# Kernel tuning notes

Hardware: AMD Instinct MI355X
Metric: run time of the kernel (lower is better)

Reference implementation:

```python
import jax, jax.numpy as jnp
import numpy as np

S, B, E, H, Q, T, K, N = 256, 32, 768, 1024, 64, 512, 11, 16
STD = 2.5
EPS = 1e-5


def gaussian_kernel(size, std):
    t = np.linspace(-(size - 1) / 2, (size - 1) / 2, size)
    x, y = np.meshgrid(t, t)
    kern = np.exp(-0.5 * (x ** 2 + y ** 2) / std ** 2)
    return (kern / kern.sum()).astype(np.float32)


def setup_inputs() -> dict:
    key = jax.random.key(0)
    ks = jax.random.split(key, 24)
    s = 0.05
    inp = {
        'sentence_batch': jax.random.normal(ks[0], (S, B, E), jnp.float32),
        # forward LSTM params (torch layout: W_ih (4H,E), W_hh (4H,H), gate order i,f,g,o)
        'Wih_f': jax.random.normal(ks[1], (4 * H, E), jnp.float32) * s,
        'Whh_f': jax.random.normal(ks[2], (4 * H, H), jnp.float32) * s,
        'bih_f': jnp.zeros((4 * H,), jnp.float32),
        'bhh_f': jnp.zeros((4 * H,), jnp.float32),
        # backward LSTM params
        'Wih_b': jax.random.normal(ks[3], (4 * H, E), jnp.float32) * s,
        'Whh_b': jax.random.normal(ks[4], (4 * H, H), jnp.float32) * s,
        'bih_b': jnp.zeros((4 * H,), jnp.float32),
        'bhh_b': jnp.zeros((4 * H,), jnp.float32),
        # layer norms
        'g_in': jnp.ones((E,), jnp.float32), 'be_in': jnp.zeros((E,), jnp.float32),
        'g_fw': jnp.ones((H,), jnp.float32), 'be_fw': jnp.zeros((H,), jnp.float32),
        'g_bk': jnp.ones((H,), jnp.float32), 'be_bk': jnp.zeros((H,), jnp.float32),
        'g_sq': jnp.ones((2 * Q,), jnp.float32), 'be_sq': jnp.zeros((2 * Q,), jnp.float32),
        # squeeze + topic linears (torch layout: W (out,in))
        'Wsq': jax.random.normal(ks[5], (Q, H), jnp.float32) * s,
        'bsq': jnp.zeros((Q,), jnp.float32),
        'Wtop': jax.random.normal(ks[6], (T, 2 * Q), jnp.float32) * s,
        'btop': jnp.zeros((T,), jnp.float32),
        'gauss_kern': jnp.asarray(gaussian_kernel(K, STD)),
    }
    return inp


def layer_norm(x, g, b):
    mu = jnp.mean(x, axis=-1, keepdims=True)
    var = jnp.mean((x - mu) ** 2, axis=-1, keepdims=True)
    return g * (x - mu) * jax.lax.rsqrt(var + EPS) + b


def lstm(x, Wih, Whh, bih, bhh):
    # x: (S, B, E) -> hidden states (S, B, H). torch gate order: i, f, g, o.
    h0 = jnp.zeros((x.shape[1], Whh.shape[1]), x.dtype)
    c0 = jnp.zeros_like(h0)
    xg = jnp.einsum('sbe,ge->sbg', x, Wih) + bih  # precompute input gates

    def step(carry, xt):
        h, c = carry
        gates = xt + h @ Whh.T + bhh
        i, f, g, o = jnp.split(gates, 4, axis=-1)
        c = jax.nn.sigmoid(f) * c + jax.nn.sigmoid(i) * jnp.tanh(g)
        h = jax.nn.sigmoid(o) * jnp.tanh(c)
        return (h, c), h

    _, hs = jax.lax.scan(step, (h0, c0), xg)
    return hs


def batch_pca(e, dim):
    # e: (S, B, F) -> projections (B, S, dim) onto top-dim principal axes
    c = e - jnp.mean(e, axis=0)
    cov = jnp.einsum('sbi,sbj->bij', c, c) / e.shape[0]  # (B, F, F), symmetric
    _, evecs = jnp.linalg.eigh(cov)  # ascending eigenvalues
    top = evecs[:, :, ::-1][:, :, :dim]  # (B, F, dim), descending order
    return jnp.einsum('sbf,bfn->bsn', c, top)


def gauss_smooth(x, kern):
    # x: (B, S, N) smoothed with 2D gaussian, SAME padding
    p = (kern.shape[0] - 1) // 2
    y = jax.lax.conv_general_dilated(
        x[:, None, :, :], kern[None, None, :, :], (1, 1), [(p, p), (p, p)])
    return y[:, 0]


def adj_cos(e):
    # cosine similarity between adjacent sequence positions: (B, S, N) -> (B, S-1)
    a, b = e[:, :-1], e[:, 1:]
    num = jnp.sum(a * b, axis=-1)
    den = jnp.linalg.norm(a, axis=-1) * jnp.linalg.norm(b, axis=-1)
    return num / den


def reference(sentence_batch, Wih_f, Whh_f, bih_f, bhh_f, Wih_b, Whh_b, bih_b, bhh_b,
              g_in, be_in, g_fw, be_fw, g_bk, be_bk, g_sq, be_sq,
              Wsq, bsq, Wtop, btop, gauss_kern):
    x = layer_norm(sentence_batch, g_in, be_in)
    x_f = lstm(x, Wih_f, Whh_f, bih_f, bhh_f)
    x_b = lstm(x[::-1], Wih_b, Whh_b, bih_b, bhh_b)[::-1]
    x_f = layer_norm(x_f, g_fw, be_fw)
    x_b = layer_norm(x_b, g_bk, be_bk)
    x_f = jnp.tanh(jnp.einsum('sbh,qh->sbq', x_f, Wsq) + bsq)
    x_b = jnp.tanh(jnp.einsum('sbh,qh->sbq', x_b, Wsq) + bsq)
    xc = layer_norm(jnp.concatenate((x_f, x_b), axis=-1), g_sq, be_sq)
    topic_preds = jnp.einsum('sbq,tq->sbt', xc, Wtop) + btop

    # segmentation path (no-grad in original)
    e_f = batch_pca(jax.lax.stop_gradient(x_f), N)
    e_b = batch_pca(jax.lax.stop_gradient(x_b), N)
    e_f = gauss_smooth(e_f, gauss_kern)
    e_b = gauss_smooth(e_b, gauss_kern)
    d = jnp.sqrt(adj_cos(e_f) * adj_cos(e_b))  # (B, S-1)
    pos = jnp.argmax(d, axis=1)
    return topic_preds, pos
```

## Files before the change

kernel.cpp:

```cpp
#include <hip/hip_runtime.h>
#include <cstdint>
#include <cstddef>

#define SS   256
#define BB   32
#define EE   768
#define HH   1024
#define QQ   64
#define TTOP 512
#define NPC  16
#define G4   4096
#define TCHUNK 32
#define NBLK 256
#define EPSF 1e-5f

#define OFF_XNT   ((size_t)0)
#define OFF_WHHT  ((size_t)6291456)
#define OFF_CT    ((size_t)14680064)
#define OFF_HBUF  ((size_t)14745600)
#define OFF_CNT   ((size_t)14876672)
#define OFF_XG    ((size_t)14877184)
#define OFF_HS    ((size_t)23265792)
#define OFF_XQ    ((size_t)40043008)
#define OFF_CMAT  ((size_t)0)
#define OFF_COV   ((size_t)1048576)
#define OFF_PG    ((size_t)1310720)
#define OFF_COS   ((size_t)1376256)

#define WLKS 4616
#define LSTM_DYN_LDS 153344

#define AST 65
#define EIG_DYN_LDS 133120

#define EPS32D    5.9604644775390625e-8
#define EPS232D   (EPS32D*EPS32D)
#define SAFMIN32D 1.1754943508222875e-38

__device__ __forceinline__ float sigm(float x){ return 1.0f/(1.0f + expf(-x)); }

__device__ __forceinline__ double wsumd(double v){
  #pragma unroll
  for (int o = 32; o; o >>= 1) v += __shfl_xor(v, o, 64);
  return v;
}
__device__ __forceinline__ double wmaxd(double v){
  #pragma unroll
  for (int o = 32; o; o >>= 1) v = fmax(v, __shfl_xor(v, o, 64));
  return v;
}
__device__ __forceinline__ void dlartg_(double f, double g, double& c, double& s, double& r){
  if (g == 0.0){ c = 1.0; s = 0.0; r = f; }
  else if (f == 0.0){ c = 0.0; s = (g >= 0.0) ? 1.0 : -1.0; r = fabs(g); }
  else {
    double d = sqrt(f*f + g*g);
    c = fabs(f)/d;
    r = copysign(d, f);
    s = g/r;
  }
}
__device__ void dlaev2_(double a, double b, double c,
                        double& rt1, double& rt2, double& cs1, double& sn1){
  double sm = a + c, df = a - c, adf = fabs(df), tb = b + b, ab = fabs(tb);
  double acmx, acmn;
  if (fabs(a) > fabs(c)){ acmx = a; acmn = c; } else { acmx = c; acmn = a; }
  double rt;
  if (adf > ab)      rt = adf*sqrt(1.0 + (ab/adf)*(ab/adf));
  else if (adf < ab) rt = ab*sqrt(1.0 + (adf/ab)*(adf/ab));
  else               rt = ab*sqrt(2.0);
  int sgn1;
  if (sm < 0.0){ rt1 = 0.5*(sm - rt); sgn1 = -1; rt2 = (acmx/rt1)*acmn - (b/rt1)*b; }
  else if (sm > 0.0){ rt1 = 0.5*(sm + rt); sgn1 = 1; rt2 = (acmx/rt1)*acmn - (b/rt1)*b; }
  else { rt1 = 0.5*rt; rt2 = -0.5*rt; sgn1 = 1; }
  double cs; int sgn2;
  if (df >= 0.0){ cs = df + rt; sgn2 = 1; } else { cs = df - rt; sgn2 = -1; }
  double acs = fabs(cs);
  if (acs > ab){ double ct = -tb/cs; sn1 = 1.0/sqrt(1.0+ct*ct); cs1 = ct*sn1; }
  else {
    if (ab == 0.0){ cs1 = 1.0; sn1 = 0.0; }
    else { double tn = -cs/tb; cs1 = 1.0/sqrt(1.0+tn*tn); sn1 = tn*cs1; }
  }
  if (sgn1 == sgn2){ double tn = cs1; cs1 = -sn1; sn1 = tn; }
}

__device__ void dsteqr16_(int base, double* d, double* e, double* z16, int ln){
  if (ln < 16){
    #pragma unroll
    for (int j = 0; j < 16; j++) z16[ln*17+j] = (ln==j) ? 1.0 : 0.0;
  }
  const int n = 16, nm1 = 15;
  int jtot = 0; const int nmaxit = 480;
  int l1 = 0;
  while (l1 < n){
    if (l1 > 0) e[base+l1-1] = 0.0;
    int m = nm1;
    for (int mm = l1; mm < nm1; mm++){
      double tst = fabs(e[base+mm]);
      if (tst == 0.0){ m = mm; break; }
      if (tst <= (sqrt(fabs(d[base+mm]))*sqrt(fabs(d[base+mm+1])))*EPS32D){
        e[base+mm] = 0.0; m = mm; break;
      }
    }
    int l = l1, lend = m;
    l1 = m + 1;
    if (lend == l) continue;
    if (fabs(d[base+lend]) < fabs(d[base+l])){ int t = l; l = lend; lend = t; }
    if (lend > l){
      for (;;){
        int mm = lend;
        for (int k2 = l; k2 < lend; k2++){
          double tst = e[base+k2]*e[base+k2];
          if (tst <= (EPS232D*fabs(d[base+k2]))*fabs(d[base+k2+1]) + SAFMIN32D){ mm = k2; break; }
        }
        if (mm < lend) e[base+mm] = 0.0;
        double p = d[base+l];
        if (mm == l){ l++; if (l <= lend) continue; break; }
        if (mm == l+1){
          double rt1, rt2, cc, ss;
          dlaev2_(d[base+l], e[base+l], d[base+l+1], rt1, rt2, cc, ss);
          if (ln < 16){
            double x = z16[ln*17+l], y = z16[ln*17+l+1];
            z16[ln*17+l]   = cc*x + ss*y;
            z16[ln*17+l+1] = cc*y - ss*x;
          }
          d[base+l] = rt1; d[base+l+1] = rt2; e[base+l] = 0.0;
          l += 2; if (l <= lend) continue; break;
        }
        if (jtot == nmaxit) break;
        jtot++;
        double g = (d[base+l+1]-p)/(2.0*e[base+l]);
        double r = sqrt(g*g+1.0);
        g = d[base+mm] - p + e[base+l]/(g + copysign(r, g));
        double s2 = 1.0, c2 = 1.0; p = 0.0;
        for (int i = mm-1; i >= l; i--){
          double f = s2*e[base+i], b = c2*e[base+i];
          dlartg_(g, f, c2, s2, r);
          if (i != mm-1) e[base+i+1] = r;
          g = d[base+i+1] - p;
          r = (d[base+i]-g)*s2 + 2.0*c2*b;
          p = s2*r;
          d[base+i+1] = g + p;
          g = c2*r - b;
          if (ln < 16){
            double x = z16[ln*17+i], y = z16[ln*17+i+1];
            z16[ln*17+i]   = c2*x - s2*y;
            z16[ln*17+i+1] = s2*x + c2*y;
          }
        }
        d[base+l] -= p; e[base+l] = g;
      }
    } else {
      for (;;){
        int mm = lend;
        for (int k2 = l; k2 > lend; k2--){
          double tst = e[base+k2-1]*e[base+k2-1];
          if (tst <= (EPS232D*fabs(d[base+k2]))*fabs(d[base+k2-1]) + SAFMIN32D){ mm = k2; break; }
        }
        if (mm > lend) e[base+mm-1] = 0.0;
        double p = d[base+l];
        if (mm == l){ l--; if (l >= lend) continue; break; }
        if (mm == l-1){
          double rt1, rt2, cc, ss;
          dlaev2_(d[base+l-1], e[base+l-1], d[base+l], rt1, rt2, cc, ss);
          if (ln < 16){
            double x = z16[ln*17+l-1], y = z16[ln*17+l];
            z16[ln*17+l-1] = cc*x + ss*y;
            z16[ln*17+l]   = cc*y - ss*x;
          }
          d[base+l-1] = rt1; d[base+l] = rt2; e[base+l-1] = 0.0;
          l -= 2; if (l >= lend) continue; break;
        }
        if (jtot == nmaxit) break;
        jtot++;
        double g = (d[base+l-1]-p)/(2.0*e[base+l-1]);
        double r = sqrt(g*g+1.0);
        g = d[base+mm] - p + e[base+l-1]/(g + copysign(r, g));
        double s2 = 1.0, c2 = 1.0; p = 0.0;
        for (int i = mm; i <= l-1; i++){
          double f = s2*e[base+i], b = c2*e[base+i];
          dlartg_(g, f, c2, s2, r);
          if (i != mm) e[base+i-1] = r;
          g = d[base+i] - p;
          r = (d[base+i+1]-g)*s2 + 2.0*c2*b;
          p = s2*r;
          d[base+i] = g + p;
          g = c2*r - b;
          if (ln < 16){
            double x = z16[ln*17+i], y = z16[ln*17+i+1];
            z16[ln*17+i]   = c2*x + s2*y;
            z16[ln*17+i+1] = c2*y - s2*x;
          }
        }
        d[base+l] -= p; e[base+l-1] = g;
      }
    }
  }
  for (int ii = 1; ii < n; ii++){
    int i = ii-1, k = i; double p = d[base+i];
    for (int j = ii; j < n; j++) if (d[base+j] < p){ k = j; p = d[base+j]; }
    if (k != i){
      d[base+k] = d[base+i]; d[base+i] = p;
      if (ln < 16){ double t = z16[ln*17+i]; z16[ln*17+i] = z16[ln*17+k]; z16[ln*17+k] = t; }
    }
  }
}

__device__ void dc_merge(int base, int n1, int n2, double rho_in, int tid,
    double* s_d, double* Zt, double* Tt,
    double* md, double* mz, double* dl, double* wz, double* lam, double* zh,
    double* ev, double* su4, int* indx, int* sec, int* defl, int* prm,
    int* sKn){
  const int ln = tid & 63, w = tid >> 6;
  int n = n1 + n2;
  double zv = 0.0;
  if (ln < n){
    if (ln < n1) zv = Zt[(size_t)(base+n1-1)*AST + base + ln];
    else         zv = Zt[(size_t)(base+n1)*AST + base + ln];
    if (rho_in < 0.0 && ln >= n1) zv = -zv;
  }
  zv *= 0.70710678118654752440;
  mz[ln] = (ln < n) ? zv : 0.0;
  md[ln] = (ln < n) ? s_d[base+ln] : 0.0;
  __syncthreads();
  double rho = fabs(2.0*rho_in);
  if (tid == 0){
    int i1 = 0, i2 = n1, k = 0;
    while (i1 < n1 && i2 < n){
      if (md[i2] < md[i1]) indx[k++] = i2++; else indx[k++] = i1++;
    }
    while (i1 < n1) indx[k++] = i1++;
    while (i2 < n)  indx[k++] = i2++;
  }
  __syncthreads();
  double dmax = wmaxd((ln<n) ? fabs(md[ln]) : 0.0);
  double zmax = wmaxd((ln<n) ? fabs(mz[ln]) : 0.0);
  double tol = 8.0*EPS32D*fmax(dmax, zmax);
  if (w == 0){
    int K = 0, ndefl = 0, pj = -1;
    for (int j = 0; j < n; j++){
      int nj = indx[j];
      if (rho*fabs(mz[nj]) <= tol){
        defl[ndefl++] = nj;
      } else if (pj < 0){
        pj = nj;
      } else {
        double sG = mz[pj], cG = mz[nj];
        double tau = sqrt(cG*cG + sG*sG);
        double tdf = md[nj] - md[pj];
        double c = cG/tau, s = -sG/tau;
        if (fabs(tdf*c*s) <= tol){
          mz[nj] = tau; mz[pj] = 0.0;
          if (ln < n){
            double x = Zt[(size_t)(base+ln)*AST + base+pj];
            double y = Zt[(size_t)(base+ln)*AST + base+nj];
            Zt[(size_t)(base+ln)*AST + base+pj] = c*x + s*y;
            Zt[(size_t)(base+ln)*AST + base+nj] = c*y - s*x;
          }
          double t2 = md[pj]*c*c + md[nj]*s*s;
          double t3 = md[pj]*s*s + md[nj]*c*c;
          md[nj] = t3; md[pj] = t2;
          defl[ndefl++] = pj;
          pj = nj;
        } else {
          sec[K] = pj; dl[K] = md[pj]; wz[K] = mz[pj]; K++;
          pj = nj;
        }
      }
    }
    if (pj >= 0){ sec[K] = pj; dl[K] = md[pj]; wz[K] = mz[pj]; K++; }
    if (ln == 0){ sKn[0] = K; sKn[1] = ndefl; }
  }
  __syncthreads();
  const int K = sKn[0], ndefl = sKn[1];
  double wsum2 = wsumd((ln < K) ? wz[ln]*wz[ln] : 0.0);
  {
    bool conv = (ln >= K);
    double lo = 0.0, hi = 0.0;
    if (!conv){
      lo = dl[ln];
      hi = (ln < K-1) ? dl[ln+1] : (dl[K-1] + rho*wsum2);
    }
    const int i2lo = w*16;
    for (int it = 0; it < 120; it++){
      double mid = 0.0;
      if (!conv){
        mid = 0.5*(lo+hi);
        if (!(mid > lo) || !(mid < hi)) conv = true;
      }
      double fp = 0.0;
      if (!conv){
        int i2hi = i2lo + 16; if (i2hi > K) i2hi = K;
        for (int i2 = i2lo; i2 < i2hi; i2++)
          fp += rho*wz[i2]*wz[i2]/(dl[i2]-mid);
      }
      su4[w*64 + ln] = fp;
      int alldone = __syncthreads_count(conv ? 1 : 0);
      if (alldone == 256) break;
      if (!conv){
        double fv = 1.0 + su4[ln] + su4[64+ln] + su4[128+ln] + su4[192+ln];
        if (fv < 0.0) lo = mid; else hi = mid;
      }
      __syncthreads();
    }
    if (ln < K){
      double lj = 0.5*(lo+hi);
      if (!(lj > dl[ln])) lj = nextafter(dl[ln], 1.0e300);
      lam[ln] = lj;
    }
  }
  __syncthreads();
  if (ln < K){
    double di = dl[ln];
    double prod = lam[K-1] - di;
    for (int j2 = 0; j2 < ln; j2++)   prod *= (lam[j2]-di)/(dl[j2]-di);
    for (int j2 = ln; j2 < K-1; j2++) prod *= (lam[j2]-di)/(dl[j2+1]-di);
    zh[ln] = copysign(sqrt(fabs(prod)), wz[ln]);
  }
  __syncthreads();
  for (int j = w; j < K; j += 4){
    double ui = (ln < K) ? zh[ln]/(dl[ln]-lam[j]) : 0.0;
    double nrm = sqrt(wsumd(ui*ui));
    su4[w*64 + ln] = ui/nrm;
    if (ln < n){
      double acc = 0.0;
      for (int i2 = 0; i2 < K; i2++)
        acc += Zt[(size_t)(base+ln)*AST + base + sec[i2]]*su4[w*64 + i2];
      Tt[(size_t)ln*AST + j] = acc;
    }
    if (ln == 0) ev[j] = lam[j];
  }
  __syncthreads();
  for (int j = 0; j < ndefl; j++){
    int cj = defl[j];
    if (ln < n) Tt[(size_t)ln*AST + K + j] = Zt[(size_t)(base+ln)*AST + base + cj];
    if (ln == 0) ev[K+j] = md[cj];
  }
  __syncthreads();
  if (tid == 0){
    for (int i2 = 0; i2 < n; i2++) prm[i2] = i2;
    for (int a2 = 0; a2 < n-1; a2++){
      int kk = a2;
      for (int b2 = a2+1; b2 < n; b2++) if (ev[prm[b2]] < ev[prm[kk]]) kk = b2;
      int t3 = prm[a2]; prm[a2] = prm[kk]; prm[kk] = t3;
    }
  }
  __syncthreads();
  if (ln < n){
    for (int c2 = 0; c2 < n; c2++)
      Zt[(size_t)(base+ln)*AST + base + c2] = Tt[(size_t)ln*AST + prm[c2]];
  }
  if (ln == 0){ for (int c2 = 0; c2 < n; c2++) s_d[base+c2] = ev[prm[c2]]; }
  __syncthreads();
}

__global__ __launch_bounds__(256) void k_eig(const float* __restrict__ covg,
                                             float* __restrict__ Pg){
  int u = blockIdx.x, tid = threadIdx.x;
  const int ln = tid & 63, w = tid >> 6;
  extern __shared__ double dsm[];
  double* A  = dsm;
  double* Qh = dsm + 4160;
  double* Zt = dsm + 8320;
  double* Tt = dsm + 12480;
  __shared__ double s_d[64], s_e[64], s_tau[64], s_v[64], s_w[64];
  __shared__ double md[64], mz[64], dl[64], wz[64], lam[64], zh[64], ev[64];
  __shared__ double su4[4*64];
  __shared__ double z16a[4*272];
  __shared__ int indx[64], sec[64], defl[64], prm[64], sKn[2];

  for (int n = tid; n < 4096; n += 256)
    A[(n >> 6)*AST + (n & 63)] = (double)covg[(size_t)u*4096 + n];
  __syncthreads();

  for (int i = 0; i < 63; i++){
    double alpha = A[(size_t)(i+1)*AST + i];
    double xv = (ln >= i+2) ? A[(size_t)ln*AST + i] : 0.0;
    double xnorm2 = wsumd(xv*xv);
    if (xnorm2 == 0.0){
      if (tid == 0){ s_e[i] = alpha; s_tau[i] = 0.0; }
    } else {
      double beta = -copysign(sqrt(alpha*alpha + xnorm2), alpha);
      double taui = (beta - alpha)/beta;
      double sc = 1.0/(alpha - beta);
      s_v[ln] = (ln == i+1) ? 1.0 : ((ln >= i+2) ? A[(size_t)ln*AST+i]*sc : 0.0);
      __syncthreads();
      if (ln >= i+2) A[(size_t)ln*AST+i] = s_v[ln];
      double wr = 0.0;
      if (ln >= i+1){
        for (int c2 = i+1; c2 < 64; c2++){
          double av = (ln >= c2) ? A[(size_t)ln*AST+c2] : A[(size_t)c2*AST+ln];
          wr += av*s_v[c2];
        }
        wr *= taui;
      }
      double dotwv = wsumd((ln >= i+1) ? wr*s_v[ln] : 0.0);
      double alp2 = -0.5*taui*dotwv;
      wr += alp2*s_v[ln];
      s_w[ln] = (ln >= i+1) ? wr : 0.0;
      __syncthreads();
      if (ln >= i+1){
        for (int c2 = i+1; c2 <= ln; c2++)
          if ((c2 & 3) == w)
            A[(size_t)ln*AST+c2] -= s_v[ln]*s_w[c2] + s_w[ln]*s_v[c2];
      }
      if (tid == 0){ s_e[i] = beta; s_tau[i] = taui; }
    }
    __syncthreads();
  }
  if (w == 0) s_d[ln] = A[(size_t)ln*AST+ln];
  __syncthreads();

  for (int n = tid; n < 4160; n += 256) Qh[n] = 0.0;
  __syncthreads();
  if (w == 0) Qh[(size_t)ln*AST+ln] = 1.0;
  __syncthreads();
  for (int i = 62; i >= 0; i--){
    double taui = s_tau[i];
    if (taui != 0.0){
      s_v[ln] = (ln == i+1) ? 1.0 : ((ln >= i+2) ? A[(size_t)ln*AST+i] : 0.0);
      __syncthreads();
      double dj = 0.0;
      for (int r2 = i+1; r2 < 64; r2++) dj += s_v[r2]*Qh[(size_t)r2*AST+ln];
      dj *= taui;
      for (int r2 = i+1; r2 < 64; r2++)
        if ((r2 & 3) == w)
          Qh[(size_t)r2*AST+ln] -= s_v[r2]*dj;
    }
    __syncthreads();
  }

  double rho_a = s_e[15], rho_b = s_e[47], rho_top = s_e[31];
  if (tid == 0){
    s_d[15] -= fabs(rho_a);   s_d[16] -= fabs(rho_a);
    s_d[31] -= fabs(rho_top); s_d[32] -= fabs(rho_top);
    s_d[47] -= fabs(rho_b);   s_d[48] -= fabs(rho_b);
  }
  for (int n = tid; n < 4160; n += 256) Zt[n] = 0.0;
  __syncthreads();
  dsteqr16_(w*16, s_d, s_e, &z16a[w*272], ln);
  if (ln < 16){
    for (int j = 0; j < 16; j++)
      Zt[(size_t)(w*16+ln)*AST + w*16 + j] = z16a[w*272 + ln*17+j];
  }
  __syncthreads();

  dc_merge(0, 16, 16, rho_a, tid, s_d, Zt, Tt, md, mz, dl, wz, lam, zh, ev, su4, indx, sec, defl, prm, sKn);
  dc_merge(32, 16, 16, rho_b, tid, s_d, Zt, Tt, md, mz, dl, wz, lam, zh, ev, su4, indx, sec, defl, prm, sKn);
  dc_merge(0, 32, 32, rho_top, tid, s_d, Zt, Tt, md, mz, dl, wz, lam, zh, ev, su4, indx, sec, defl, prm, sKn);

  for (int nn = w; nn < 16; nn += 4){
    double acc = 0.0;
    for (int k = 0; k < 64; k++)
      acc += Qh[(size_t)ln*AST+k]*Zt[(size_t)k*AST + (63-nn)];
    Pg[(size_t)u*1024 + ln*16 + nn] = (float)acc;
  }
}

__global__ void k_ln_in(const float* __restrict__ x, const float* __restrict__ g,
                        const float* __restrict__ be, float* __restrict__ xnT){
  int bid = blockIdx.x; int s = bid >> 5, b = bid & 31;
  int tid = threadIdx.x;
  const float* row = x + ((size_t)(s*BB + b))*EE;
  __shared__ float r1[256], r2[256];
  float su = 0.f, sq = 0.f;
  for (int e = tid; e < EE; e += 256){ float v = row[e]; su += v; sq += v*v; }
  r1[tid] = su; r2[tid] = sq; __syncthreads();
  for (int st = 128; st > 0; st >>= 1){
    if (tid < st){ r1[tid] += r1[tid+st]; r2[tid] += r2[tid+st]; }
    __syncthreads();
  }
  float mu  = r1[0] * (1.0f/EE);
  float var = r2[0] * (1.0f/EE) - mu*mu;
  float rstd = rsqrtf(var + EPSF);
  for (int e = tid; e < EE; e += 256){
    float v = (row[e]-mu)*rstd*g[e] + be[e];
    xnT[((size_t)s*EE + e)*BB + b] = v;
  }
}

__global__ void k_whht(const float* __restrict__ Whh_f, const float* __restrict__ Whh_b,
                       float* __restrict__ WhhT){
  int d  = blockIdx.z;
  const float* Whh = d ? Whh_b : Whh_f;
  int rt = blockIdx.x*32, kt = blockIdx.y*32;
  int tx = threadIdx.x & 31, ty = threadIdx.x >> 5;
  __shared__ float tile[32][33];
  for (int i = ty; i < 32; i += 8)
    tile[i][tx] = Whh[(size_t)(rt+i)*HH + kt+tx];
  __syncthreads();
  for (int i = ty; i < 32; i += 8)
    WhhT[((size_t)d*HH + kt+i)*G4 + rt+tx] = tile[tx][i];
}

__global__ void k_zero(float* __restrict__ p, int n){
  int i = blockIdx.x*blockDim.x + threadIdx.x;
  if (i < n) p[i] = 0.f;
}

__global__ __launch_bounds__(256) void k_xg(const float* __restrict__ xnT,
        const float* __restrict__ Wih_f, const float* __restrict__ Wih_b,
        float* __restrict__ xg, int* __restrict__ cnt, int c){
  if (blockIdx.x == 0 && blockIdx.y == 0){
    if (threadIdx.x < 17)
      __hip_atomic_store(&cnt[threadIdx.x*16], 0, __ATOMIC_RELAXED, __HIP_MEMORY_SCOPE_AGENT);
    else if (threadIdx.x == 17)
      __hip_atomic_store(&cnt[384], 0, __ATOMIC_RELAXED, __HIP_MEMORY_SCOPE_AGENT);
  }
  int nb = blockIdx.x, rb = blockIdx.y;
  int d = rb >> 5, rloc0 = (rb & 31)*128;
  const float* Wih = d ? Wih_b : Wih_f;
  int tid = threadIdx.x;
  int tx = tid & 15, ty = tid >> 4;
  __shared__ float Al[16*132];
  __shared__ float Bl[16*132];
  float acc[8][8];
  #pragma unroll
  for (int i = 0; i < 8; i++)
    #pragma unroll
    for (int j = 0; j < 8; j++) acc[i][j] = 0.f;
  for (int kc = 0; kc < EE; kc += 16){
    #pragma unroll
    for (int j = 0; j < 8; j++){
      int idx = tid + j*256;
      int n = idx & 127, k = idx >> 7;
      int tglob = c*TCHUNK + nb*4 + (n >> 5);
      int tsrc = d ? (SS-1-tglob) : tglob;
      Al[k*132 + n] = xnT[((size_t)tsrc*EE + kc + k)*BB + (n & 31)];
    }
    #pragma unroll
    for (int j = 0; j < 8; j++){
      int idx = tid + j*256;
      int k = idx & 15, r = idx >> 4;
      Bl[k*132 + r] = Wih[(size_t)(rloc0 + r)*EE + kc + k];
    }
    __syncthreads();
    #pragma unroll
    for (int k = 0; k < 16; k++){
      float4 a0 = *(const float4*)(&Al[k*132 + tx*4]);
      float4 a1 = *(const float4*)(&Al[k*132 + 64 + tx*4]);
      float4 b0 = *(const float4*)(&Bl[k*132 + ty*4]);
      float4 b1 = *(const float4*)(&Bl[k*132 + 64 + ty*4]);
      float av[8] = {a0.x,a0.y,a0.z,a0.w,a1.x,a1.y,a1.z,a1.w};
      float bv[8] = {b0.x,b0.y,b0.z,b0.w,b1.x,b1.y,b1.z,b1.w};
      #pragma unroll
      for (int i = 0; i < 8; i++)
        #pragma unroll
        for (int j2 = 0; j2 < 8; j2++) acc[i][j2] += av[i]*bv[j2];
    }
    __syncthreads();
  }
  #pragma unroll
  for (int j = 0; j < 8; j++){
    int r = rloc0 + ((j < 4) ? (ty*4 + j) : (64 + ty*4 + j - 4));
    #pragma unroll
    for (int ig = 0; ig < 2; ig++){
      int n0 = ig*64 + tx*4;
      int tl = nb*4 + (n0 >> 5), b = n0 & 31;
      float4 o = make_float4(acc[ig*4+0][j], acc[ig*4+1][j], acc[ig*4+2][j], acc[ig*4+3][j]);
      *(float4*)(&xg[(((size_t)tl*8192) + d*G4 + r)*BB + b]) = o;
    }
  }
}

__global__ __launch_bounds__(512) void k_lstm(
    const float* __restrict__ WhhT,
    const float* __restrict__ bih_f, const float* __restrict__ bhh_f,
    const float* __restrict__ bih_b, const float* __restrict__ bhh_b,
    const float* __restrict__ xg, float* __restrict__ hbuf,
    float* __restrict__ cT, float* __restrict__ hs,
    int* __restrict__ cnt, int c)
{
  extern __shared__ float lsm[];
  float* Wl  = lsm;
  float* gl  = lsm + 36928;
  float* cls = lsm + 38080;

  const int blk = blockIdx.x;
  const int d   = blk >> 7;
  const int j0  = (blk & 127) * 8;
  const int tid = threadIdx.x;
  const int ln  = tid & 63;
  const int w   = tid >> 6;
  const int ksub = ln >> 3;
  const int bg   = ln & 7;
  const int b0   = bg * 4;
  const int cbase = w * 4;

  const float* bih = d ? bih_b : bih_f;
  const float* bhh = d ? bhh_b : bhh_f;
  const float* WT_d = WhhT + (size_t)d * HH * G4;

  {
    const int cs = tid & 31;
    const int ks = tid >> 5;
    const int g  = cs >> 3, jj = cs & 7;
    const size_t rglob = (size_t)g*HH + j0 + jj;
    for (int kk = 0; kk < 64; kk++){
      int k = kk*16 + ks;
      Wl[(k >> 7)*WLKS + (k & 127)*36 + cs] = WT_d[(size_t)k*G4 + rglob];
    }
  }

  const int pjj = (tid >> 5) & 7, pb = tid & 31;
  float pbias[4];
  if (tid < 256){
    cls[pjj*32 + pb] = cT[((size_t)d*HH + j0 + pjj)*BB + pb];
    #pragma unroll
    for (int g2 = 0; g2 < 4; g2++)
      pbias[g2] = bih[g2*HH + j0 + pjj] + bhh[g2*HH + j0 + pjj];
  }
  __syncthreads();

  for (int tl = 0; tl < TCHUNK; tl++){
    const int s = c*TCHUNK + tl;
    const float* hprev = hbuf + ((size_t)((s & 1)*2 + d))*HH*BB;
    float*       hnext = hbuf + ((size_t)(((s+1) & 1)*2 + d))*HH*BB;

    float xgv[4] = {0.f,0.f,0.f,0.f};
    if (tid < 256){
      const size_t xbase = ((size_t)tl*8192 + (size_t)d*G4)*BB;
      #pragma unroll
      for (int g2 = 0; g2 < 4; g2++)
        xgv[g2] = xg[xbase + (size_t)(g2*HH + j0 + pjj)*BB + pb];
    }

    float acc[4][4];
    #pragma unroll
    for (int i = 0; i < 4; i++)
      #pragma unroll
      for (int j = 0; j < 4; j++) acc[i][j] = 0.f;

    {
      const float* hp = hprev + (size_t)(ksub*128)*BB + b0;
      const float* wrow = &Wl[ksub*WLKS + cbase];
      for (int ib = 0; ib < 128; ib += 16){
        float4 hv[16];
        #pragma unroll
        for (int u = 0; u < 16; u++)
          hv[u] = *(const float4*)(hp + (size_t)(ib+u)*BB);
        #pragma unroll
        for (int u = 0; u < 16; u++){
          float4 wv = *(const float4*)(wrow + (ib+u)*36);
          acc[0][0] += wv.x*hv[u].x; acc[0][1] += wv.x*hv[u].y; acc[0][2] += wv.x*hv[u].z; acc[0][3] += wv.x*hv[u].w;
          acc[1][0] += wv.y*hv[u].x; acc[1][1] += wv.y*hv[u].y; acc[1][2] += wv.y*hv[u].z; acc[1][3] += wv.y*hv[u].w;
          acc[2][0] += wv.z*hv[u].x; acc[2][1] += wv.z*hv[u].y; acc[2][2] += wv.z*hv[u].z; acc[2][3] += wv.z*hv[u].w;
          acc[3][0] += wv.w*hv[u].x; acc[3][1] += wv.w*hv[u].y; acc[3][2] += wv.w*hv[u].z; acc[3][3] += wv.w*hv[u].w;
        }
      }
    }
    #pragma unroll
    for (int i = 0; i < 4; i++)
      #pragma unroll
      for (int j = 0; j < 4; j++){
        float v = acc[i][j];
        v += __shfl_xor(v, 8, 64);
        v += __shfl_xor(v, 16, 64);
        v += __shfl_xor(v, 32, 64);
        acc[i][j] = v;
      }
    if (ksub == 0){
      #pragma unroll
      for (int i = 0; i < 4; i++){
        float4 o = make_float4(acc[i][0], acc[i][1], acc[i][2], acc[i][3]);
        *(float4*)(&gl[(cbase + i)*36 + b0]) = o;
      }
    }
    __syncthreads();
    if (tid < 256){
      float gv[4];
      #pragma unroll
      for (int g2 = 0; g2 < 4; g2++)
        gv[g2] = gl[(g2*8 + pjj)*36 + pb] + pbias[g2] + xgv[g2];
      float iv = sigm(gv[0]), fv = sigm(gv[1]), ggv = tanhf(gv[2]), ov = sigm(gv[3]);
      float cv = fv*cls[pjj*32 + pb] + iv*ggv;
      cls[pjj*32 + pb] = cv;
      float h = ov*tanhf(cv);
      hnext[(size_t)(j0 + pjj)*BB + pb] = h;
      int tsv = d ? (SS-1-s) : s;
      hs[(((size_t)d*SS + tsv)*HH + j0 + pjj)*BB + pb] = h;
    }
    if (tl < TCHUNK-1){
      __syncthreads();
      if (tid == 0){
        __builtin_amdgcn_fence(__ATOMIC_RELEASE, "agent");
        __hip_atomic_fetch_add(&cnt[((blk & 7) + d*8)*16], 1, __ATOMIC_RELAXED, __HIP_MEMORY_SCOPE_AGENT);
        const int target = 16*(tl+1);
        const int flagidx = d ? 384 : 256;
        if ((blk & 127) == 0){
          const int lbase = d*8;
          int done = 0;
          while (done < 8){
            done = 0;
            #pragma unroll
            for (int i = 0; i < 8; i++)
              done += (__hip_atomic_load(&cnt[(lbase+i)*16], __ATOMIC_RELAXED, __HIP_MEMORY_SCOPE_AGENT) >= target);
            if (done < 8) __builtin_amdgcn_s_sleep(2);
          }
          __hip_atomic_store(&cnt[flagidx], tl+1, __ATOMIC_RELAXED, __HIP_MEMORY_SCOPE_AGENT);
        } else {
          while (__hip_atomic_load(&cnt[flagidx], __ATOMIC_RELAXED, __HIP_MEMORY_SCOPE_AGENT) < tl+1)
            __builtin_amdgcn_s_sleep(2);
        }
        __builtin_amdgcn_fence(__ATOMIC_ACQUIRE, "agent");
      }
      __syncthreads();
    }
  }
  __syncthreads();
  if (tid < 256)
    cT[((size_t)d*HH + j0 + pjj)*BB + pb] = cls[pjj*32 + pb];
}

__global__ __launch_bounds__(256) void k_lnproj(const float* __restrict__ hs,
        const float* __restrict__ g_fw, const float* __restrict__ be_fw,
        const float* __restrict__ g_bk, const float* __restrict__ be_bk,
        const float* __restrict__ Wsq, const float* __restrict__ bsq,
        float* __restrict__ xq){
  int t = blockIdx.x, d = blockIdx.y;
  int tid = threadIdx.x;
  const float* gv  = d ? g_bk  : g_fw;
  const float* bev = d ? be_bk : be_fw;
  const float* hrow = hs + ((size_t)d*SS + t)*HH*BB;
  __shared__ float red[256], red2[256];
  __shared__ float smu[32], srs[32];
  __shared__ float ln[32*132];
  __shared__ float wl[64*132];
  {
    int b = tid & 31, jg = tid >> 5;
    float s = 0.f, s2 = 0.f;
    for (int j = jg*128; j < jg*128+128; j++){
      float v = hrow[(size_t)j*BB + b];
      s += v; s2 += v*v;
    }
    red[b*8 + jg] = s; red2[b*8 + jg] = s2; __syncthreads();
    if (tid < 32){
      float a = 0.f, a2 = 0.f;
      for (int k = 0; k < 8; k++){ a += red[tid*8+k]; a2 += red2[tid*8+k]; }
      float mu = a*(1.f/HH), var = a2*(1.f/HH) - mu*mu;
      smu[tid] = mu; srs[tid] = rsqrtf(var + EPSF);
    }
    __syncthreads();
  }
  float acc[4][2] = {{0.f,0.f},{0.f,0.f},{0.f,0.f},{0.f,0.f}};
  int qg = tid & 31, bg = tid >> 5;
  int q0 = qg*2, b0g = bg*4;
  for (int jc = 0; jc < 8; jc++){
    for (int n = tid; n < 4096; n += 256){
      int b = n & 31, jj = n >> 5; int j = jc*128 + jj;
      float v = hrow[(size_t)j*BB + b];
      ln[b*132+jj] = (v - smu[b])*srs[b]*gv[j] + bev[j];
    }
    for (int n = tid; n < 8192; n += 256){
      int q = n >> 7, jj = n & 127;
      wl[q*132+jj] = Wsq[(size_t)q*HH + jc*128 + jj];
    }
    __syncthreads();
    for (int jj = 0; jj < 128; jj += 4){
      float4 w0 = *(const float4*)(&wl[q0*132+jj]);
      float4 w1 = *(const float4*)(&wl[(q0+1)*132+jj]);
      #pragma unroll
      for (int i = 0; i < 4; i++){
        float4 xv = *(const float4*)(&ln[(b0g+i)*132+jj]);
        acc[i][0] += xv.x*w0.x + xv.y*w0.y + xv.z*w0.z + xv.w*w0.w;
        acc[i][1] += xv.x*w1.x + xv.y*w1.y + xv.z*w1.z + xv.w*w1.w;
      }
    }
    __syncthreads();
  }
  #pragma unroll
  for (int i = 0; i < 4; i++)
    #pragma unroll
    for (int u = 0; u < 2; u++){
      float o = tanhf(acc[i][u] + bsq[q0+u]);
      xq[(((size_t)d*SS + t)*BB + (b0g+i))*QQ + q0 + u] = o;
    }
}

__global__ __launch_bounds__(256) void k_topic(const float* __restrict__ xq,
        const float* __restrict__ g_sq, const float* __restrict__ be_sq,
        const float* __restrict__ Wtop, const float* __restrict__ btop,
        float* __restrict__ out){
  int t = blockIdx.x; int tid = threadIdx.x;
  __shared__ float xc[32*132];
  __shared__ float wl[16*520];
  __shared__ float red[256], red2[256];
  __shared__ float smu[32], srs[32];
  for (int n = tid; n < 4096; n += 256){
    int b = n >> 7, q = n & 127;
    float v = (q < 64) ? xq[(((size_t)0*SS + t)*BB + b)*QQ + q]
                       : xq[(((size_t)1*SS + t)*BB + b)*QQ + (q-64)];
    xc[b*132+q] = v;
  }
  __syncthreads();
  {
    int b = tid >> 3, sl = tid & 7;
    float s = 0.f, s2 = 0.f;
    for (int k = 0; k < 16; k++){ float v = xc[b*132 + sl*16 + k]; s += v; s2 += v*v; }
    red[tid] = s; red2[tid] = s2; __syncthreads();
    if (tid < 32){
      float a = 0.f, a2 = 0.f;
      for (int k = 0; k < 8; k++){ a += red[tid*8+k]; a2 += red2[tid*8+k]; }
      float mu = a*(1.f/128.f), var = a2*(1.f/128.f) - mu*mu;
      smu[tid] = mu; srs[tid] = rsqrtf(var + EPSF);
    }
    __syncthreads();
    for (int n = tid; n < 4096; n += 256){
      int b2 = n >> 7, q = n & 127;
      xc[b2*132+q] = (xc[b2*132+q]-smu[b2])*srs[b2]*g_sq[q] + be_sq[q];
    }
    __syncthreads();
  }
  int og = tid & 63, bg = tid >> 6;
  int o0 = og*8, b0 = bg*8;
  float acc[8][8];
  #pragma unroll
  for (int i = 0; i < 8; i++)
    #pragma unroll
    for (int j = 0; j < 8; j++) acc[i][j] = 0.f;
  for (int kc = 0; kc < 128; kc += 16){
    for (int n = tid; n < 8192; n += 256){
      int o = n >> 4, kk = n & 15;
      wl[kk*520 + o] = Wtop[(size_t)o*128 + kc + kk];
    }
    __syncthreads();
    #pragma unroll
    for (int kk = 0; kk < 16; kk++){
      float4 w0 = *(const float4*)(&wl[kk*520+o0]);
      float4 w1 = *(const float4*)(&wl[kk*520+o0+4]);
      float wv[8] = {w0.x,w0.y,w0.z,w0.w,w1.x,w1.y,w1.z,w1.w};
      int k = kc + kk;
      #pragma unroll
      for (int bi = 0; bi < 8; bi++){
        float xv = xc[(b0+bi)*132 + k];
        #pragma unroll
        for (int oi = 0; oi < 8; oi++) acc[bi][oi] += xv*wv[oi];
      }
    }
    __syncthreads();
  }
  #pragma unroll
  for (int bi = 0; bi < 8; bi++){
    int b = b0 + bi;
    #pragma unroll
    for (int oi = 0; oi < 8; oi++)
      out[((size_t)t*BB + b)*TTOP + o0 + oi] = acc[bi][oi] + btop[o0+oi];
  }
}

__global__ __launch_bounds__(256) void k_pca1(const float* __restrict__ xq,
        float* __restrict__ cmat, float* __restrict__ covg){
  int u = blockIdx.x; int d = u >> 5, b = u & 31;
  int tid = threadIdx.x;
  __shared__ float red[256];
  __shared__ float smq[64];
  {
    int q = tid & 63, tg = tid >> 6;
    float s = 0.f;
    for (int t2 = tg*64; t2 < tg*64+64; t2++)
      s += xq[(((size_t)d*SS + t2)*BB + b)*QQ + q];
    red[tid] = s; __syncthreads();
    if (tid < 64) smq[tid] = (red[tid]+red[tid+64]+red[tid+128]+red[tid+192])*(1.f/SS);
    __syncthreads();
  }
  float* cm = cmat + (size_t)u*SS*QQ;
  for (int n = tid; n < SS*QQ; n += 256){
    int t2 = n >> 6, q = n & 63;
    cm[n] = xq[(((size_t)d*SS + t2)*BB + b)*QQ + q] - smq[q];
  }
  __syncthreads();
  {
    int pg = (tid & 15)*4, qg = (tid >> 4)*4;
    float a[4][4] = {{0}};
    for (int t2 = 0; t2 < SS; t2++){
      const float* cr = cm + (size_t)t2*QQ;
      float4 cp = *(const float4*)(cr+pg);
      float4 cq = *(const float4*)(cr+qg);
      float pv[4] = {cp.x,cp.y,cp.z,cp.w}, qv[4] = {cq.x,cq.y,cq.z,cq.w};
      #pragma unroll
      for (int i = 0; i < 4; i++)
        #pragma unroll
        for (int j2 = 0; j2 < 4; j2++) a[i][j2] += pv[i]*qv[j2];
    }
    #pragma unroll
    for (int i = 0; i < 4; i++)
      #pragma unroll
      for (int j2 = 0; j2 < 4; j2++)
        covg[(size_t)u*4096 + (pg+i)*64 + qg+j2] = a[i][j2]*(1.f/SS);
  }
}

__global__ __launch_bounds__(256) void k_pca2(const float* __restrict__ cmat,
        const float* __restrict__ Pg, const float* __restrict__ kern,
        float* __restrict__ cosb){
  int u = blockIdx.x; int tid = threadIdx.x;
  __shared__ float sP[1024];
  __shared__ float sE[4096];
  __shared__ float sY[4096];
  __shared__ float kb[121];
  __shared__ float nn2[256];
  if (tid < 121) kb[tid] = kern[tid];
  for (int n = tid; n < 1024; n += 256) sP[n] = Pg[(size_t)u*1024 + n];
  __syncthreads();
  const float* cm = cmat + (size_t)u*SS*QQ;
  for (int m = tid; m < SS*NPC; m += 256){
    int t2 = m >> 4, n = m & 15;
    const float* cr = cm + (size_t)t2*QQ;
    float acc = 0.f;
    for (int i = 0; i < 64; i++) acc += cr[i]*sP[i*16+n];
    sE[m] = acc;
  }
  __syncthreads();
  for (int m = tid; m < SS*NPC; m += 256){
    int t2 = m >> 4, n = m & 15;
    float acc = 0.f;
    for (int a2 = 0; a2 < 11; a2++){
      int ta = t2 + a2 - 5;
      if (ta < 0 || ta >= SS) continue;
      #pragma unroll
      for (int b2 = 0; b2 < 11; b2++){
        int nb = n + b2 - 5;
        if (nb < 0 || nb >= NPC) continue;
        acc += kb[a2*11+b2]*sE[ta*16+nb];
      }
    }
    sY[m] = acc;
  }
  __syncthreads();
  {
    float acc = 0.f;
    #pragma unroll
    for (int n = 0; n < 16; n++){ float v = sY[tid*16+n]; acc += v*v; }
    nn2[tid] = acc;
  }
  __syncthreads();
  if (tid < 255){
    float num = 0.f;
    #pragma unroll
    for (int n = 0; n < 16; n++) num += sY[tid*16+n]*sY[(tid+1)*16+n];
    cosb[(size_t)u*256 + tid] = num/(sqrtf(nn2[tid])*sqrtf(nn2[tid+1]));
  }
}

__global__ void k_pos(const float* __restrict__ cosb, float* __restrict__ out){
  __shared__ float mx[256];
  __shared__ int   mi[256];
  int tid = threadIdx.x;
  for (int b = 0; b < 32; b++){
    float v = -1e30f;
    if (tid < 255){
      float cf = cosb[(size_t)(b)*256 + tid];
      float cb = cosb[(size_t)(32+b)*256 + tid];
      v = sqrtf(cf*cb);
      if (isnan(v)) v = INFINITY;
    }
    mx[tid] = v; __syncthreads();
    for (int st = 128; st > 0; st >>= 1){
      if (tid < st) mx[tid] = fmaxf(mx[tid], mx[tid+st]);
      __syncthreads();
    }
    float m = mx[0]; __syncthreads();
    mi[tid] = (tid < 255 && v == m) ? tid : (1<<30);
    __syncthreads();
    for (int st = 128; st > 0; st >>= 1){
      if (tid < st) mi[tid] = min(mi[tid], mi[tid+st]);
      __syncthreads();
    }
    if (tid == 0) out[(size_t)SS*BB*TTOP + b] = (float)mi[0];
    __syncthreads();
  }
}

extern "C" void kernel_launch(void* const* d_in, const int* in_sizes, int n_in,
                              void* d_out, int out_size, void* d_ws, size_t ws_size,
                              hipStream_t stream){
  (void)in_sizes; (void)n_in; (void)out_size; (void)ws_size;
  const float* x      = (const float*)d_in[0];
  const float* Wih_f  = (const float*)d_in[1];
  const float* Whh_f  = (const float*)d_in[2];
  const float* bih_f  = (const float*)d_in[3];
  const float* bhh_f  = (const float*)d_in[4];
  const float* Wih_b  = (const float*)d_in[5];
  const float* Whh_b  = (const float*)d_in[6];
  const float* bih_b  = (const float*)d_in[7];
  const float* bhh_b  = (const float*)d_in[8];
  const float* g_in   = (const float*)d_in[9];
  const float* be_in  = (const float*)d_in[10];
  const float* g_fw   = (const float*)d_in[11];
  const float* be_fw  = (const float*)d_in[12];
  const float* g_bk   = (const float*)d_in[13];
  const float* be_bk  = (const float*)d_in[14];
  const float* g_sq   = (const float*)d_in[15];
  const float* be_sq  = (const float*)d_in[16];
  const float* Wsq    = (const float*)d_in[17];
  const float* bsq    = (const float*)d_in[18];
  const float* Wtop   = (const float*)d_in[19];
  const float* btop   = (const float*)d_in[20];
  const float* gkern  = (const float*)d_in[21];

  float* ws    = (float*)d_ws;
  float* xnT   = ws + OFF_XNT;
  float* WhhT  = ws + OFF_WHHT;
  float* cT    = ws + OFF_CT;
  float* hbuf  = ws + OFF_HBUF;
  int*   cnt   = (int*)(ws + OFF_CNT);
  float* xg    = ws + OFF_XG;
  float* hs    = ws + OFF_HS;
  float* xq    = ws + OFF_XQ;
  float* cmat  = ws + OFF_CMAT;
  float* covg  = ws + OFF_COV;
  float* Pg    = ws + OFF_PG;
  float* cosb  = ws + OFF_COS;
  float* out   = (float*)d_out;

  hipFuncSetAttribute((const void*)k_eig,
                      hipFuncAttributeMaxDynamicSharedMemorySize, EIG_DYN_LDS);
  hipFuncSetAttribute((const void*)k_lstm,
                      hipFuncAttributeMaxDynamicSharedMemorySize, LSTM_DYN_LDS);

  k_zero<<<dim3(768), dim3(256), 0, stream>>>(cT, 196608);
  k_ln_in<<<dim3(SS*BB), dim3(256), 0, stream>>>(x, g_in, be_in, xnT);
  k_whht<<<dim3(128, 32, 2), dim3(256), 0, stream>>>(Whh_f, Whh_b, WhhT);
  for (int c = 0; c < SS/TCHUNK; c++){
    k_xg<<<dim3(8, 64), dim3(256), 0, stream>>>(xnT, Wih_f, Wih_b, xg, cnt, c);
    k_lstm<<<dim3(NBLK), dim3(512), LSTM_DYN_LDS, stream>>>(WhhT, bih_f, bhh_f, bih_b, bhh_b,
                                                            xg, hbuf, cT, hs, cnt, c);
  }
  k_lnproj<<<dim3(SS,2), dim3(256), 0, stream>>>(hs, g_fw, be_fw, g_bk, be_bk, Wsq, bsq, xq);
  k_topic<<<dim3(SS), dim3(256), 0, stream>>>(xq, g_sq, be_sq, Wtop, btop, out);
  k_pca1<<<dim3(64), dim3(256), 0, stream>>>(xq, cmat, covg);
  k_eig<<<dim3(64), dim3(256), EIG_DYN_LDS, stream>>>(covg, Pg);
  k_pca2<<<dim3(64), dim3(256), 0, stream>>>(cmat, Pg, gkern, cosb);
  k_pos<<<dim3(1), dim3(256), 0, stream>>>(cosb, out);
}
```

Before: 7.489 ms.

## Run first-level eigen merges concurrently per wavefront; replace serial sorts with rank sort

The two 16+16 divide-and-conquer merges in the per-batch eigensolver now run concurrently, one wavefront each, through a new barrier-free single-wave merge routine. The serial selection sorts in the 16x16 QL solver and in the merge permutation are replaced by parallel rank-based sorts. The secular-equation bisection double-buffers its shared partial sums so one barrier per iteration can be dropped. This targets serialized single-thread work and barrier overhead in the eigen kernel, but that kernel is probably a small share of total time, which is likely dominated by the LSTM.

```diff
diff --git a/kernel.cpp b/kernel.cpp
--- a/kernel.cpp
+++ b/kernel.cpp
@@ -83,7 +83,8 @@
   if (sgn1 == sgn2){ double tn = cs1; cs1 = -sn1; sn1 = tn; }
 }
 
-__device__ void dsteqr16_(int base, double* d, double* e, double* z16, int ln){
+__device__ void dsteqr16_(int base, double* d, double* e, double* z16, int ln,
+                          double* tmpd, double* tmpz, int* rk){
   if (ln < 16){
     #pragma unroll
     for (int j = 0; j < 16; j++) z16[ln*17+j] = (ln==j) ? 1.0 : 0.0;
@@ -195,13 +196,131 @@
       }
     }
   }
-  for (int ii = 1; ii < n; ii++){
-    int i = ii-1, k = i; double p = d[base+i];
-    for (int j = ii; j < n; j++) if (d[base+j] < p){ k = j; p = d[base+j]; }
-    if (k != i){
-      d[base+k] = d[base+i]; d[base+i] = p;
-      if (ln < 16){ double t = z16[ln*17+i]; z16[ln*17+i] = z16[ln*17+k]; z16[ln*17+k] = t; }
-    }
+  if (ln < 16){
+    double di = d[base+ln]; int r = 0;
+    for (int j = 0; j < 16; j++){
+      double dj = d[base+j];
+      if (dj < di || (dj == di && j < ln)) r++;
+    }
+    rk[ln] = r;
+    tmpd[r] = di;
+  }
+  if (ln < 16){
+    for (int j = 0; j < 16; j++) tmpz[ln*16 + rk[j]] = z16[ln*17 + j];
+    for (int j = 0; j < 16; j++) z16[ln*17 + j] = tmpz[ln*16 + j];
+    d[base+ln] = tmpd[ln];
+  }
+}
+
+__device__ void dc_merge1(int base, int n1, int n2, double rho_in, int ln,
+    double* s_d, double* Zt, double* Ttp,
+    double* md, double* mz, double* dl, double* wz, double* lam, double* zh,
+    double* ev, double* su, int* indx, int* sec, int* defl, int* prm){
+  const int n = n1 + n2;
+  double zv = 0.0;
+  if (ln < n){
+    if (ln < n1) zv = Zt[(size_t)(base+n1-1)*AST + base + ln];
+    else         zv = Zt[(size_t)(base+n1)*AST + base + ln];
+    if (rho_in < 0.0 && ln >= n1) zv = -zv;
+  }
+  zv *= 0.70710678118654752440;
+  double mdv = (ln < n) ? s_d[base+ln] : 0.0;
+  if (ln < n){ mz[ln] = zv; md[ln] = mdv; }
+  double rho = fabs(2.0*rho_in);
+  if (ln == 0){
+    int i1 = 0, i2 = n1, k = 0;
+    while (i1 < n1 && i2 < n){
+      if (md[i2] < md[i1]) indx[k++] = i2++; else indx[k++] = i1++;
+    }
+    while (i1 < n1) indx[k++] = i1++;
+    while (i2 < n)  indx[k++] = i2++;
+  }
+  double dmax = wmaxd((ln<n) ? fabs(mdv) : 0.0);
+  double zmax = wmaxd((ln<n) ? fabs(zv) : 0.0);
+  double tol = 8.0*EPS32D*fmax(dmax, zmax);
+  int K = 0, ndefl = 0, pj = -1;
+  for (int j = 0; j < n; j++){
+    int nj = indx[j];
+    if (rho*fabs(mz[nj]) <= tol){
+      defl[ndefl++] = nj;
+    } else if (pj < 0){
+      pj = nj;
+    } else {
+      double sG = mz[pj], cG = mz[nj];
+      double tau = sqrt(cG*cG + sG*sG);
+      double tdf = md[nj] - md[pj];
+      double c = cG/tau, s = -sG/tau;
+      if (fabs(tdf*c*s) <= tol){
+        mz[nj] = tau; mz[pj] = 0.0;
+        if (ln < n){
+          double x = Zt[(size_t)(base+ln)*AST + base+pj];
+          double y = Zt[(size_t)(base+ln)*AST + base+nj];
+          Zt[(size_t)(base+ln)*AST + base+pj] = c*x + s*y;
+          Zt[(size_t)(base+ln)*AST + base+nj] = c*y - s*x;
+        }
+        double t2 = md[pj]*c*c + md[nj]*s*s;
+        double t3 = md[pj]*s*s + md[nj]*c*c;
+        md[nj] = t3; md[pj] = t2;
+        defl[ndefl++] = pj;
+        pj = nj;
+      } else {
+        sec[K] = pj; dl[K] = md[pj]; wz[K] = mz[pj]; K++;
+        pj = nj;
+      }
+    }
+  }
+  if (pj >= 0){ sec[K] = pj; dl[K] = md[pj]; wz[K] = mz[pj]; K++; }
+  double wsum2 = wsumd((ln < K) ? wz[ln]*wz[ln] : 0.0);
+  if (ln < K){
+    double lo = dl[ln];
+    double hi = (ln < K-1) ? dl[ln+1] : (dl[K-1] + rho*wsum2);
+    for (int it = 0; it < 120; it++){
+      double mid = 0.5*(lo+hi);
+      if (!(mid > lo) || !(mid < hi)) break;
+      double fv = 1.0;
+      for (int i2 = 0; i2 < K; i2++) fv += rho*wz[i2]*wz[i2]/(dl[i2]-mid);
+      if (fv < 0.0) lo = mid; else hi = mid;
+    }
+    double lj = 0.5*(lo+hi);
+    if (!(lj > dl[ln])) lj = nextafter(dl[ln], 1.0e300);
+    lam[ln] = lj;
+  }
+  if (ln < K){
+    double di = dl[ln];
+    double prod = lam[K-1] - di;
+    for (int j2 = 0; j2 < ln; j2++)   prod *= (lam[j2]-di)/(dl[j2]-di);
+    for (int j2 = ln; j2 < K-1; j2++) prod *= (lam[j2]-di)/(dl[j2+1]-di);
+    zh[ln] = copysign(sqrt(fabs(prod)), wz[ln]);
+  }
+  for (int j = 0; j < K; j++){
+    double ui = (ln < K) ? zh[ln]/(dl[ln]-lam[j]) : 0.0;
+    double nrm = sqrt(wsumd(ui*ui));
+    su[ln] = ui/nrm;
+    if (ln < n){
+      double acc = 0.0;
+      for (int i2 = 0; i2 < K; i2++)
+        acc += Zt[(size_t)(base+ln)*AST + base + sec[i2]]*su[i2];
+      Ttp[(size_t)ln*AST + j] = acc;
+    }
+    ev[j] = lam[j];
+  }
+  for (int j = 0; j < ndefl; j++){
+    int cj = defl[j];
+    if (ln < n) Ttp[(size_t)ln*AST + K + j] = Zt[(size_t)(base+ln)*AST + base + cj];
+    ev[K+j] = md[cj];
+  }
+  if (ln < n){
+    double di = ev[ln]; int r = 0;
+    for (int j2 = 0; j2 < n; j2++){
+      double dj = ev[j2];
+      if (dj < di || (dj == di && j2 < ln)) r++;
+    }
+    prm[r] = ln;
+  }
+  if (ln < n){
+    for (int c2 = 0; c2 < n; c2++)
+      Zt[(size_t)(base+ln)*AST + base + c2] = Ttp[(size_t)ln*AST + prm[c2]];
+    s_d[base+ln] = ev[prm[ln]];
   }
 }
 
@@ -293,14 +412,14 @@
         for (int i2 = i2lo; i2 < i2hi; i2++)
           fp += rho*wz[i2]*wz[i2]/(dl[i2]-mid);
       }
-      su4[w*64 + ln] = fp;
+      const int p = (it & 1)*256;
+      su4[p + w*64 + ln] = fp;
       int alldone = __syncthreads_count(conv ? 1 : 0);
       if (alldone == 256) break;
       if (!conv){
-        double fv = 1.0 + su4[ln] + su4[64+ln] + su4[128+ln] + su4[192+ln];
+        double fv = 1.0 + su4[p+ln] + su4[p+64+ln] + su4[p+128+ln] + su4[p+192+ln];
         if (fv < 0.0) lo = mid; else hi = mid;
       }
-      __syncthreads();
     }
     if (ln < K){
       double lj = 0.5*(lo+hi);
@@ -336,13 +455,13 @@
     if (ln == 0) ev[K+j] = md[cj];
   }
   __syncthreads();
-  if (tid == 0){
-    for (int i2 = 0; i2 < n; i2++) prm[i2] = i2;
-    for (int a2 = 0; a2 < n-1; a2++){
-      int kk = a2;
-      for (int b2 = a2+1; b2 < n; b2++) if (ev[prm[b2]] < ev[prm[kk]]) kk = b2;
-      int t3 = prm[a2]; prm[a2] = prm[kk]; prm[kk] = t3;
-    }
+  if (w == 0 && ln < n){
+    double di = ev[ln]; int r = 0;
+    for (int j2 = 0; j2 < n; j2++){
+      double dj = ev[j2];
+      if (dj < di || (dj == di && j2 < ln)) r++;
+    }
+    prm[r] = ln;
   }
   __syncthreads();
   if (ln < n){
@@ -364,7 +483,7 @@
   double* Tt = dsm + 12480;
   __shared__ double s_d[64], s_e[64], s_tau[64], s_v[64], s_w[64];
   __shared__ double md[64], mz[64], dl[64], wz[64], lam[64], zh[64], ev[64];
-  __shared__ double su4[4*64];
+  __shared__ double su4[2*4*64];
   __shared__ double z16a[4*272];
   __shared__ int indx[64], sec[64], defl[64], prm[64], sKn[2];
 
@@ -437,15 +556,24 @@
   }
   for (int n = tid; n < 4160; n += 256) Zt[n] = 0.0;
   __syncthreads();
-  dsteqr16_(w*16, s_d, s_e, &z16a[w*272], ln);
+  dsteqr16_(w*16, s_d, s_e, &z16a[w*272], ln,
+            &su4[w*64], Tt + (size_t)w*1040, &indx[w*16]);
   if (ln < 16){
     for (int j = 0; j < 16; j++)
       Zt[(size_t)(w*16+ln)*AST + w*16 + j] = z16a[w*272 + ln*17+j];
   }
   __syncthreads();
 
-  dc_merge(0, 16, 16, rho_a, tid, s_d, Zt, Tt, md, mz, dl, wz, lam, zh, ev, su4, indx, sec, defl, prm, sKn);
-  dc_merge(32, 16, 16, rho_b, tid, s_d, Zt, Tt, md, mz, dl, wz, lam, zh, ev, su4, indx, sec, defl, prm, sKn);
+  if (w == 0)
+    dc_merge1(0, 16, 16, rho_a, ln, s_d, Zt, Tt,
+              md, mz, dl, wz, lam, zh, ev, su4,
+              indx, sec, defl, prm);
+  else if (w == 1)
+    dc_merge1(32, 16, 16, rho_b, ln, s_d, Zt, Tt + (size_t)32*AST,
+              md+32, mz+32, dl+32, wz+32, lam+32, zh+32, ev+32, su4+64,
+              indx+32, sec+32, defl+32, prm+32);
+  __syncthreads();
+
   dc_merge(0, 32, 32, rho_top, tid, s_d, Zt, Tt, md, mz, dl, wz, lam, zh, ev, su4, indx, sec, defl, prm, sKn);
 
   for (int nn = w; nn < 16; nn += 4){
```

Result: faster. 7.268 ms (-3.0%).
